# Performance work log

Measured on AMD Instinct MI355X. Metric: run time of the kernel, lower is better.

The kernel has to match this reference:

```python
import jax, jax.numpy as jnp
import numpy as np

HEAD_NUM = 16
NEG_BIG = 1e12


def setup_inputs() -> dict:
    key = jax.random.key(0)
    ks = jax.random.split(key, 10)
    B, S, H = 4, 2048, 1024
    std = 0.02
    return {
        "encoder_outputs": jax.random.normal(ks[0], (B, S, H), dtype=jnp.float32),
        "mask": jax.random.randint(ks[1], (B, S), 0, 2, dtype=jnp.int32),
        "Wq": jax.random.normal(ks[2], (H, H), dtype=jnp.float32) * std,
        "bq": jax.random.normal(ks[3], (H,), dtype=jnp.float32) * std,
        "Wk": jax.random.normal(ks[4], (H, H), dtype=jnp.float32) * std,
        "bk": jax.random.normal(ks[5], (H,), dtype=jnp.float32) * std,
        "Wv": jax.random.normal(ks[6], (H, H), dtype=jnp.float32) * std,
        "bv": jax.random.normal(ks[7], (H,), dtype=jnp.float32) * std,
        "Wc": jax.random.normal(ks[8], (H, H), dtype=jnp.float32) * std,
    }


def _split_heads(x, h):
    # chunk(h, -1) + stack(dim=0): [B,S,H] -> [h,B,S,H//h]
    B, S, H = x.shape
    return jnp.moveaxis(x.reshape(B, S, h, H // h), 2, 0)


def reference(encoder_outputs, mask, Wq, bq, Wk, bk, Wv, bv, Wc):
    x = encoder_outputs
    B, S, H = x.shape
    hd = H // HEAD_NUM
    q = _split_heads(x @ Wq.T + bq, HEAD_NUM)  # [h,B,S,hd]
    k = _split_heads(x @ Wk.T + bk, HEAD_NUM)
    v = _split_heads(x @ Wv.T + bv, HEAD_NUM)
    dots = jnp.einsum("hbqd,hbkd->hbqk", q, k) / jnp.sqrt(jnp.float32(hd))
    m = mask.astype(jnp.float32)  # [B,S]; 0 = valid token
    inv = 1.0 - m
    eye = jnp.eye(S, dtype=jnp.float32)
    # clamp_max(1 - (1-m)_i (1-m)_j + eye, 1): [B,S,S]
    new_mask = jnp.minimum(1.0 - inv[:, :, None] * inv[:, None, :] + eye, 1.0)
    energies = dots - new_mask[None] * NEG_BIG
    weights = jax.nn.softmax(energies, axis=-1) * (1.0 - new_mask)[None]
    out = jnp.einsum("hbqk,hbkd->hbqd", weights, v)  # [h,B,S,hd]
    out = jnp.moveaxis(out, 0, 2).reshape(B, S, H)  # concat heads
    return out @ Wc.T
```

## Files before the change

### kernel.cpp

```cpp
#include <hip/hip_runtime.h>
#include <cstddef>
#include <cstdint>

#define BB 4
#define SS 2048
#define HH 1024
#define NH 16
#define HD 64

typedef _Float16 half8 __attribute__((ext_vector_type(8)));
typedef _Float16 half4v __attribute__((ext_vector_type(4)));
typedef float f32x4 __attribute__((ext_vector_type(4)));

#define KSCALE 0.1803368801111f

__device__ __forceinline__ void gload_lds16(const _Float16* g, char* l) {
    __builtin_amdgcn_global_load_lds(
        (const __attribute__((address_space(1))) void*)g,
        (__attribute__((address_space(3))) void*)l, 16, 0, 0);
}

__global__ __launch_bounds__(256)
void scan_mask(const int* __restrict__ mk, int* __restrict__ vidx, int* __restrict__ cnt)
{
    __shared__ int ps[256];
    const int b = blockIdx.x, t = threadIdx.x;
    int flag[8], s = 0;
#pragma unroll
    for (int k = 0; k < 8; ++k) { flag[k] = (mk[(b << 11) + t * 8 + k] == 0); s += flag[k]; }
    ps[t] = s;
    __syncthreads();
    for (int off = 1; off < 256; off <<= 1) {
        const int add = (t >= off) ? ps[t - off] : 0;
        __syncthreads();
        ps[t] += add;
        __syncthreads();
    }
    int pos = ps[t] - s;
#pragma unroll
    for (int k = 0; k < 8; ++k)
        if (flag[k]) vidx[(b << 11) + pos++] = t * 8 + k;
    if (t == 255) cnt[b] = ps[255];
}

__global__ __launch_bounds__(256)
void gather_x(const float* __restrict__ x, const int* __restrict__ vidx,
              const int* __restrict__ cnt, _Float16* __restrict__ xc)
{
    const int row = blockIdx.x;
    const int b = row >> 11, i = row & 2047;
    const int t = threadIdx.x;
    half4v hv = (half4v){0, 0, 0, 0};
    if (i < cnt[b]) {
        const float4 v = ((const float4*)(x + (size_t)((b << 11) + vidx[row]) * HH))[t];
        hv[0] = (_Float16)v.x; hv[1] = (_Float16)v.y;
        hv[2] = (_Float16)v.z; hv[3] = (_Float16)v.w;
    }
    ((half4v*)(xc + (size_t)row * HH))[t] = hv;
}

__global__ __launch_bounds__(256)
void cvt_w(const float* __restrict__ Wq, const float* __restrict__ Wk,
           const float* __restrict__ Wv, const float* __restrict__ Wc,
           _Float16* __restrict__ o)
{
    const float* src = blockIdx.z == 0 ? Wq : blockIdx.z == 1 ? Wk :
                       blockIdx.z == 2 ? Wv : Wc;
    _Float16* dst = o + (size_t)blockIdx.z * (HH * HH);
    const int i = blockIdx.x * 256 + threadIdx.x;
    const float4 v0 = ((const float4*)src)[(size_t)i * 2];
    const float4 v1 = ((const float4*)src)[(size_t)i * 2 + 1];
    half8 hv;
    hv[0] = (_Float16)v0.x; hv[1] = (_Float16)v0.y;
    hv[2] = (_Float16)v0.z; hv[3] = (_Float16)v0.w;
    hv[4] = (_Float16)v1.x; hv[5] = (_Float16)v1.y;
    hv[6] = (_Float16)v1.z; hv[7] = (_Float16)v1.w;
    ((half8*)dst)[i] = hv;
}

__device__ __forceinline__ void gemm_core(const _Float16* __restrict__ A,
                                          const _Float16* __restrict__ W,
                                          int K, int m0, int n0,
                                          char* As, char* Bs, f32x4 acc[4][4])
{
    const int t = threadIdx.x;
    const int w = t >> 6, lane = t & 63;
    const int ln = lane & 15, g = lane >> 4;
    const int wr = w >> 1, wc = w & 1;

    const int rr0 = w * 16 + (lane >> 2);
    const int rr1 = rr0 + 64;
    const int p   = lane & 3;
    const int sl0 = p ^ ((rr0 >> 1) & 3);
    const int sl1 = p ^ ((rr1 >> 1) & 3);
    const _Float16* ga0 = A + (size_t)(m0 + rr0) * K + sl0 * 8;
    const _Float16* ga1 = A + (size_t)(m0 + rr1) * K + sl1 * 8;
    const _Float16* gb0 = W + (size_t)(n0 + rr0) * K + sl0 * 8;
    const _Float16* gb1 = W + (size_t)(n0 + rr1) * K + sl1 * 8;
    char* dA = As + w * 1024 + lane * 16;
    char* dB = Bs + w * 1024 + lane * 16;

    int offA[4], offB[4];
#pragma unroll
    for (int i = 0; i < 4; ++i) {
        const int ra = wr * 64 + i * 16 + ln;
        offA[i] = ra * 64 + ((g ^ ((ra >> 1) & 3)) << 4);
        const int rb = wc * 64 + i * 16 + ln;
        offB[i] = rb * 64 + ((g ^ ((rb >> 1) & 3)) << 4);
    }

#pragma unroll
    for (int i = 0; i < 4; ++i)
#pragma unroll
        for (int j = 0; j < 4; ++j) acc[i][j] = (f32x4){0.f, 0.f, 0.f, 0.f};

    gload_lds16(ga0, dA);
    gload_lds16(ga1, dA + 4096);
    gload_lds16(gb0, dB);
    gload_lds16(gb1, dB + 4096);
    gload_lds16(ga0 + 32, dA + 8192);
    gload_lds16(ga1 + 32, dA + 8192 + 4096);
    gload_lds16(gb0 + 32, dB + 8192);
    gload_lds16(gb1 + 32, dB + 8192 + 4096);

    const int ns = K / 32;
    for (int k = 0; k < ns; ++k) {
        if (k < ns - 1) { asm volatile("s_waitcnt vmcnt(4)" ::: "memory"); }
        else            { asm volatile("s_waitcnt vmcnt(0)" ::: "memory"); }
        __builtin_amdgcn_s_barrier();
        __builtin_amdgcn_sched_barrier(0);

        const char* Ab = As + ((k & 1) << 13);
        const char* Bb = Bs + ((k & 1) << 13);
        half8 af[4], bf[4];
#pragma unroll
        for (int i = 0; i < 4; ++i) af[i] = *(const half8*)(Ab + offA[i]);
#pragma unroll
        for (int j = 0; j < 4; ++j) bf[j] = *(const half8*)(Bb + offB[j]);

        asm volatile("s_waitcnt lgkmcnt(0)" ::: "memory");
        __builtin_amdgcn_s_barrier();
        __builtin_amdgcn_sched_barrier(0);

        if (k + 2 < ns) {
            const int nb = (k & 1) << 13;
            const int ko = (k + 2) * 32;
            gload_lds16(ga0 + ko, dA + nb);
            gload_lds16(ga1 + ko, dA + nb + 4096);
            gload_lds16(gb0 + ko, dB + nb);
            gload_lds16(gb1 + ko, dB + nb + 4096);
        }
#pragma unroll
        for (int i = 0; i < 4; ++i)
#pragma unroll
            for (int j = 0; j < 4; ++j)
                acc[i][j] = __builtin_amdgcn_mfma_f32_16x16x32_f16(af[i], bf[j], acc[i][j], 0, 0, 0);
    }
}

__global__ __launch_bounds__(256)
void gemm_qkv(const _Float16* __restrict__ xc,
              const _Float16* __restrict__ Wq16, const _Float16* __restrict__ Wk16,
              const _Float16* __restrict__ Wv16,
              const float* __restrict__ bq, const float* __restrict__ bk,
              const float* __restrict__ bv, const int* __restrict__ cnt,
              _Float16* __restrict__ Qh, _Float16* __restrict__ Kh,
              _Float16* __restrict__ Vt)
{
    const int m0 = blockIdx.y * 128;
    const int bI = m0 >> 11;
    if ((m0 & 2047) >= ((cnt[bI] + 127) & ~127)) return;

    __shared__ __align__(16) char As[16384];
    __shared__ __align__(16) char Bs[16384];
    const int z = blockIdx.z;
    const _Float16* W = (z == 0) ? Wq16 : (z == 1) ? Wk16 : Wv16;
    const float* bias = (z == 0) ? bq : (z == 1) ? bk : bv;
    const int n0 = blockIdx.x * 128;

    f32x4 acc[4][4];
    gemm_core(xc, W, HH, m0, n0, As, Bs, acc);

    const int t = threadIdx.x;
    const int w = t >> 6, lane = t & 63;
    const int ln = lane & 15, g = lane >> 4;
    const int wr = w >> 1, wc = w & 1;
    const int mBase = m0 + wr * 64 + g * 4;
    const int nBase = n0 + wc * 64 + ln;

    if (z < 2) {
        _Float16* O = z ? Kh : Qh;
        const float sc = z ? 1.0f : KSCALE;
#pragma unroll
        for (int j = 0; j < 4; ++j) {
            const int n = nBase + j * 16;
            const int h = n >> 6, d = n & 63;
            const float bvf = bias[n];
#pragma unroll
            for (int i = 0; i < 4; ++i) {
                const int m = mBase + i * 16;
                const int b = m >> 11, s = m & 2047;
                _Float16* dst = O + (((size_t)(b * NH + h) * SS + s) * HD + d);
#pragma unroll
                for (int r = 0; r < 4; ++r)
                    dst[(size_t)r * HD] = (_Float16)((acc[i][j][r] + bvf) * sc);
            }
        }
    } else {
#pragma unroll
        for (int j = 0; j < 4; ++j) {
            const int n = nBase + j * 16;
            const int h = n >> 6, d = n & 63;
            const float bvf = bias[n];
#pragma unroll
            for (int i = 0; i < 4; ++i) {
                const int m = mBase + i * 16;
                const int b = m >> 11, s = m & 2047;
                half4v v;
#pragma unroll
                for (int r = 0; r < 4; ++r) v[r] = (_Float16)(acc[i][j][r] + bvf);
                *(half4v*)(Vt + ((size_t)(b * NH + h) * HD + d) * SS + s) = v;
            }
        }
    }
}

__global__ __launch_bounds__(256)
void gemm_out(const _Float16* __restrict__ Oc, const _Float16* __restrict__ Wc16,
              const int* __restrict__ cnt, const int* __restrict__ vidx,
              float* __restrict__ C)
{
    const int m0 = blockIdx.y * 128;
    const int bI = m0 >> 11;
    const int cb = cnt[bI];
    if ((m0 & 2047) >= ((cb + 127) & ~127)) return;

    __shared__ __align__(16) char As[16384];
    __shared__ __align__(16) char Bs[16384];
    const int n0 = blockIdx.x * 128;

    f32x4 acc[4][4];
    gemm_core(Oc, Wc16, HH, m0, n0, As, Bs, acc);

    const int t = threadIdx.x;
    const int w = t >> 6, lane = t & 63;
    const int ln = lane & 15, g = lane >> 4;
    const int wr = w >> 1, wc = w & 1;
    const int mBase = m0 + wr * 64 + g * 4;
    const int nBase = n0 + wc * 64 + ln;
#pragma unroll
    for (int i = 0; i < 4; ++i) {
#pragma unroll
        for (int r = 0; r < 4; ++r) {
            const int m = mBase + i * 16 + r;
            const int lm = m & 2047;
            if (lm < cb) {
                const int orig = vidx[m];
                const size_t off = (size_t)((m & ~2047) + orig) * HH + nBase;
#pragma unroll
                for (int j = 0; j < 4; ++j)
                    C[off + j * 16] = acc[i][j][r];
            }
        }
    }
}

__global__ __launch_bounds__(512, 4)
void attn_mfma(const _Float16* __restrict__ Qh, const _Float16* __restrict__ Kh,
               const _Float16* __restrict__ Vt, const int* __restrict__ cnt,
               _Float16* __restrict__ Oc)
{
    __shared__ __align__(16) char ksm[2][8192];
    __shared__ __align__(16) char vsm[2][8192];

    const int t  = threadIdx.x;
    const int w  = t >> 6, l = t & 63, ln = l & 15, g = l >> 4;
    const int bh = blockIdx.x;
    const int b  = bh >> 4, h = bh & 15;
    const int cb = cnt[b];
    const int q0 = blockIdx.y << 7;
    if (q0 >= cb) return;
    const int qw = q0 + (w << 4);
    const bool active = (qw < cb);
    const int nt = (cb + 63) >> 6;
    const int jtd = qw >> 6;
    const int qoff = qw & 63;

    half8 qf[2];
    f32x4 oacc[4];
    float lrun = 0.f;
    if (active) {
        const int qg = qw + ln;
        const _Float16* qp = Qh + ((size_t)bh * SS + qg) * HD + g * 8;
        qf[0] = *(const half8*)qp;
        qf[1] = *(const half8*)(qp + 32);
#pragma unroll
        for (int dd = 0; dd < 4; ++dd) oacc[dd] = (f32x4){0.f, 0.f, 0.f, 0.f};
    }

    const int sr = t >> 3;
    const int sl = (t & 7) ^ (sr & 7);
    const _Float16* kbase = Kh + ((size_t)bh * SS + sr) * HD + sl * 8;
    const _Float16* vbase = Vt + ((size_t)bh * HD + sr) * SS + sl * 8;

    gload_lds16(kbase, ksm[0] + t * 16);
    gload_lds16(vbase, vsm[0] + t * 16);
    __syncthreads();

    int buf = 0;
    for (int jt = 0; jt < nt; ++jt) {
        const int j0 = jt << 6;
        if (jt + 1 < nt) {
            gload_lds16(kbase + (size_t)(j0 + 64) * HD, ksm[buf ^ 1] + t * 16);
            gload_lds16(vbase + (j0 + 64),              vsm[buf ^ 1] + t * 16);
        }
        if (active) {
            half8 kf[4][2];
#pragma unroll
            for (int tau = 0; tau < 4; ++tau) {
                const int row = tau * 16 + ln;
                const int sw  = (row & 7) << 4;
                const int rb  = row * 128;
                kf[tau][0] = *(const half8*)(ksm[buf] + ((rb + g * 16)      ^ sw));
                kf[tau][1] = *(const half8*)(ksm[buf] + ((rb + 64 + g * 16) ^ sw));
            }
            const bool slow = (jt == jtd) | (j0 + 64 > cb);

            f32x4 sa[4];
            __builtin_amdgcn_s_setprio(1);
#pragma unroll
            for (int tau = 0; tau < 4; ++tau) {
                sa[tau] = (f32x4){0.f, 0.f, 0.f, 0.f};
                sa[tau] = __builtin_amdgcn_mfma_f32_16x16x32_f16(kf[tau][0], qf[0], sa[tau], 0, 0, 0);
                sa[tau] = __builtin_amdgcn_mfma_f32_16x16x32_f16(kf[tau][1], qf[1], sa[tau], 0, 0, 0);
            }
            __builtin_amdgcn_s_setprio(0);

            float wv[4][4], rs = 0.f;
#pragma unroll
            for (int tau = 0; tau < 4; ++tau)
#pragma unroll
                for (int r = 0; r < 4; ++r) {
                    float tv = sa[tau][r];
                    if (slow) {
                        const int kp = tau * 16 + g * 4 + r;
                        const int rel = qoff + ln;
                        if (((jt == jtd) & (kp == rel)) | (j0 + kp >= cb))
                            tv = -1e30f;
                    }
                    const float e = exp2f(tv);
                    wv[tau][r] = e; rs += e;
                }
            lrun += rs;

            half8 pf[2];
#pragma unroll
            for (int kk = 0; kk < 2; ++kk) {
                half8 pp;
                pp[0] = (_Float16)wv[2*kk][0];     pp[1] = (_Float16)wv[2*kk][1];
                pp[2] = (_Float16)wv[2*kk][2];     pp[3] = (_Float16)wv[2*kk][3];
                pp[4] = (_Float16)wv[2*kk+1][0];   pp[5] = (_Float16)wv[2*kk+1][1];
                pp[6] = (_Float16)wv[2*kk+1][2];   pp[7] = (_Float16)wv[2*kk+1][3];
                pf[kk] = pp;
            }

            __builtin_amdgcn_s_setprio(1);
#pragma unroll
            for (int dd = 0; dd < 4; ++dd) {
                const int row = dd * 16 + ln;
                const int sw  = (row & 7) << 4;
                const int rb  = row * 128;
#pragma unroll
                for (int kk = 0; kk < 2; ++kk) {
                    half4v a0 = *(const half4v*)(vsm[buf] + ((rb + kk * 64 + g * 8)      ^ sw));
                    half4v a1 = *(const half4v*)(vsm[buf] + ((rb + kk * 64 + 32 + g * 8) ^ sw));
                    half8 vf;
                    vf[0] = a0[0]; vf[1] = a0[1]; vf[2] = a0[2]; vf[3] = a0[3];
                    vf[4] = a1[0]; vf[5] = a1[1]; vf[6] = a1[2]; vf[7] = a1[3];
                    oacc[dd] = __builtin_amdgcn_mfma_f32_16x16x32_f16(vf, pf[kk], oacc[dd], 0, 0, 0);
                }
            }
            __builtin_amdgcn_s_setprio(0);
        }
        __syncthreads();
        buf ^= 1;
    }

    if (active) {
        float ls = lrun;
        ls += __shfl_xor(ls, 16);
        ls += __shfl_xor(ls, 32);
        const int iq = qw + ln;
        if (iq < cb) {
            const float inv = (ls > 0.f) ? 1.f / ls : 0.f;
            _Float16* op = Oc + ((size_t)((b << 11) + iq)) * HH + h * HD + g * 4;
#pragma unroll
            for (int dd = 0; dd < 4; ++dd) {
                half4v hv;
#pragma unroll
                for (int r = 0; r < 4; ++r) hv[r] = (_Float16)(oacc[dd][r] * inv);
                *(half4v*)(op + dd * 16) = hv;
            }
        }
    }
}

extern "C" void kernel_launch(void* const* d_in, const int* in_sizes, int n_in,
                              void* d_out, int out_size, void* d_ws, size_t ws_size,
                              hipStream_t stream)
{
    (void)in_sizes; (void)n_in; (void)ws_size;

    const float* x  = (const float*)d_in[0];
    const int*   mk = (const int*)d_in[1];
    const float* Wq = (const float*)d_in[2];
    const float* bq = (const float*)d_in[3];
    const float* Wk = (const float*)d_in[4];
    const float* bk = (const float*)d_in[5];
    const float* Wv = (const float*)d_in[6];
    const float* bv = (const float*)d_in[7];
    const float* Wc = (const float*)d_in[8];
    float* out = (float*)d_out;

    const int M = BB * SS;
    const size_t NE = (size_t)M * HH;
    const size_t NW = (size_t)HH * HH;
    _Float16* xc  = (_Float16*)d_ws;
    _Float16* W16 = xc + NE;
    _Float16* Qh  = W16 + 4 * NW;
    _Float16* Kh  = Qh + NE;
    _Float16* Vt  = Kh + NE;
    _Float16* Oc  = Vt + NE;
    int* vidx = (int*)(Oc + NE);
    int* cnt  = vidx + M;

    hipMemsetAsync(out, 0, (size_t)out_size * sizeof(float), stream);
    scan_mask<<<BB, 256, 0, stream>>>(mk, vidx, cnt);
    gather_x<<<M, 256, 0, stream>>>(x, vidx, cnt, xc);
    cvt_w<<<dim3(512, 1, 4), 256, 0, stream>>>(Wq, Wk, Wv, Wc, W16);

    dim3 gq(HH / 128, M / 128, 3);
    gemm_qkv<<<gq, 256, 0, stream>>>(xc, W16, W16 + NW, W16 + 2 * NW,
                                     bq, bk, bv, cnt, Qh, Kh, Vt);

    dim3 ga(BB * NH, SS / 128);
    attn_mfma<<<ga, 512, 0, stream>>>(Qh, Kh, Vt, cnt, Oc);

    dim3 go(HH / 128, M / 128);
    gemm_out<<<go, 256, 0, stream>>>(Oc, W16 + 3 * NW, cnt, vidx, out);
}
```

Baseline: 142.5 us.

## Triple-buffer K/V tiles with vmcnt waits and permute Vt for single LDS reads

```diff
diff --git a/kernel.cpp b/kernel.cpp
--- a/kernel.cpp
+++ b/kernel.cpp
@@ -216,10 +216,11 @@
             for (int i = 0; i < 4; ++i) {
                 const int m = mBase + i * 16;
                 const int b = m >> 11, s = m & 2047;
+                const int sp = (s & ~31) | (((s >> 2) & 3) << 3) | (((s >> 4) & 1) << 2);
                 half4v v;
 #pragma unroll
                 for (int r = 0; r < 4; ++r) v[r] = (_Float16)(acc[i][j][r] + bvf);
-                *(half4v*)(Vt + ((size_t)(b * NH + h) * HD + d) * SS + s) = v;
+                *(half4v*)(Vt + ((size_t)(b * NH + h) * HD + d) * SS + sp) = v;
             }
         }
     }
@@ -270,8 +271,8 @@
                const _Float16* __restrict__ Vt, const int* __restrict__ cnt,
                _Float16* __restrict__ Oc)
 {
-    __shared__ __align__(16) char ksm[2][8192];
-    __shared__ __align__(16) char vsm[2][8192];
+    __shared__ __align__(16) char ksm[3][8192];
+    __shared__ __align__(16) char vsm[3][8192];
 
     const int t  = threadIdx.x;
     const int w  = t >> 6, l = t & 63, ln = l & 15, g = l >> 4;
@@ -305,24 +306,37 @@
 
     gload_lds16(kbase, ksm[0] + t * 16);
     gload_lds16(vbase, vsm[0] + t * 16);
-    __syncthreads();
-
-    int buf = 0;
+    if (nt > 1) {
+        gload_lds16(kbase + (size_t)64 * HD, ksm[1] + t * 16);
+        gload_lds16(vbase + 64,              vsm[1] + t * 16);
+    }
+
+    int cur = 0;
     for (int jt = 0; jt < nt; ++jt) {
-        const int j0 = jt << 6;
-        if (jt + 1 < nt) {
-            gload_lds16(kbase + (size_t)(j0 + 64) * HD, ksm[buf ^ 1] + t * 16);
-            gload_lds16(vbase + (j0 + 64),              vsm[buf ^ 1] + t * 16);
-        }
+        if (jt < nt - 1) { asm volatile("s_waitcnt vmcnt(2) lgkmcnt(0)" ::: "memory"); }
+        else             { asm volatile("s_waitcnt vmcnt(0) lgkmcnt(0)" ::: "memory"); }
+        __builtin_amdgcn_s_barrier();
+        __builtin_amdgcn_sched_barrier(0);
+
+        if (jt + 2 < nt) {
+            const int nb = (cur + 2 >= 3) ? cur - 1 : cur + 2;
+            const int jn = (jt + 2) << 6;
+            gload_lds16(kbase + (size_t)jn * HD, ksm[nb] + t * 16);
+            gload_lds16(vbase + jn,              vsm[nb] + t * 16);
+        }
+
         if (active) {
+            const int j0 = jt << 6;
+            const char* kb = ksm[cur];
+            const char* vb = vsm[cur];
             half8 kf[4][2];
 #pragma unroll
             for (int tau = 0; tau < 4; ++tau) {
                 const int row = tau * 16 + ln;
                 const int sw  = (row & 7) << 4;
                 const int rb  = row * 128;
-                kf[tau][0] = *(const half8*)(ksm[buf] + ((rb + g * 16)      ^ sw));
-                kf[tau][1] = *(const half8*)(ksm[buf] + ((rb + 64 + g * 16) ^ sw));
+                kf[tau][0] = *(const half8*)(kb + ((rb + g * 16)      ^ sw));
+                kf[tau][1] = *(const half8*)(kb + ((rb + 64 + g * 16) ^ sw));
             }
             const bool slow = (jt == jtd) | (j0 + 64 > cb);
 
@@ -372,18 +386,13 @@
                 const int rb  = row * 128;
 #pragma unroll
                 for (int kk = 0; kk < 2; ++kk) {
-                    half4v a0 = *(const half4v*)(vsm[buf] + ((rb + kk * 64 + g * 8)      ^ sw));
-                    half4v a1 = *(const half4v*)(vsm[buf] + ((rb + kk * 64 + 32 + g * 8) ^ sw));
-                    half8 vf;
-                    vf[0] = a0[0]; vf[1] = a0[1]; vf[2] = a0[2]; vf[3] = a0[3];
-                    vf[4] = a1[0]; vf[5] = a1[1]; vf[6] = a1[2]; vf[7] = a1[3];
+                    const half8 vf = *(const half8*)(vb + ((rb + kk * 64 + g * 16) ^ sw));
                     oacc[dd] = __builtin_amdgcn_mfma_f32_16x16x32_f16(vf, pf[kk], oacc[dd], 0, 0, 0);
                 }
             }
             __builtin_amdgcn_s_setprio(0);
         }
-        __syncthreads();
-        buf ^= 1;
+        cur = (cur + 1 == 3) ? 0 : cur + 1;
     }
 
     if (active) {
```

Result: no change. 140.2 us (-1.6%).
